# Optimization experiments

Hardware: AMD Instinct MI355X
Metric: run time of the kernel (lower is better)

The kernel has to match this reference:

```python
import jax, jax.numpy as jnp
import numpy as np
import math

B, H, S, D = 2, 16, 2048, 72
D12 = D // 12  # freq dim per head per component
L_PREFIX, L_SEQ = 576, 512
THETA_T = 100.0


def _make_freqs():
    n = H * D12
    log_min, log_max = math.log(math.pi), math.log(10.0 * math.pi)
    f = jnp.exp(jnp.linspace(log_min, log_max, n + 1)[:-1])  # (H*D12,)
    freqs = jnp.stack([f, f]).reshape(2, D12, H)
    freqs = jnp.swapaxes(freqs, -1, -2)  # (2, H, D12)
    t = THETA_T ** (-jnp.arange(n, dtype=jnp.float32) / n)
    t_freqs = t.reshape(D12, H).T  # (H, D12)
    return freqs.astype(jnp.float32), t_freqs.astype(jnp.float32)


def setup_inputs() -> dict:
    key = jax.random.key(0)
    ks = jax.random.split(key, 8)
    freqs, t_freqs = _make_freqs()
    return {
        "q": jax.random.normal(ks[0], (B, H, S, D), dtype=jnp.float32),
        "k": jax.random.normal(ks[1], (B, H, S, D), dtype=jnp.float32),
        "v": jax.random.normal(ks[2], (B, H, S, D), dtype=jnp.float32),
        "pos": jax.random.uniform(ks[3], (B, S, 2), dtype=jnp.float32),
        "pos_orig": jax.random.uniform(ks[4], (B, S, 2), dtype=jnp.float32),
        "time": jax.random.uniform(ks[5], (B, S), dtype=jnp.float32),
        "freqs": freqs,
        "t_freqs": t_freqs,
        "scale": jax.random.uniform(ks[6], (H, 1, 1), dtype=jnpp_f32()) if False else jax.random.uniform(ks[6], (H, 1, 1), dtype=jnp.float32) + 0.5,
        "l_prefix": L_PREFIX,
        "l_seq": L_SEQ,
    }


def jnp_f32():
    return jnp.float32


def _fp_rope_theta(pos, pos_orig, time, freqs, t_freqs):
    # FPRoPE.forward: theta per token, per head. (B,S,H,5*D12)
    p = jnp.stack([pos_orig, pos], axis=2) * 2.0 - 1.0  # (B,S,2,2)
    th_w = p[..., 0][:, :, :, None, None] * freqs[0]  # (B,S,2,H,D12)
    th_h = p[..., 1][:, :, :, None, None] * freqs[1]  # (B,S,2,H,D12)
    th_t = time[:, :, None, None, None] * t_freqs      # (B,S,1,H,D12)
    theta = jnp.concatenate([th_h, th_w, th_t], axis=2)  # (B,S,5,H,D12)
    theta = jnp.transpose(theta, (0, 3, 1, 2, 4)).reshape(B, H, S, 5 * D12)
    return theta


def _apply_rotary(x, theta):
    d = theta.shape[-1]
    x1, x2, x3 = x[..., :d], x[..., d:2 * d], x[..., 2 * d:]
    c, s = jnp.cos(theta), jnp.sin(theta)
    return jnp.concatenate([x1 * c - x2 * s, x2 * c + x1 * s, x3], axis=-1)


def _block_mask(l_prefix, l_seq):
    # inference_query_causal_mask_mod: prefix attends to nothing; pokes causal;
    # queries attend to prefix+pokes (and self via qn==kn).
    idx = jnp.arange(S)
    qn = (idx - l_prefix)[:, None]
    kn = (idx - l_prefix)[None, :]
    return (qn >= 0) & ((qn == kn) | ((qn >= kn) & (qn < l_seq)) | ((kn < l_seq) & (qn >= l_seq)))


def reference(q, k, v, pos, pos_orig, time, freqs, t_freqs, scale, l_prefix, l_seq):
    theta = _fp_rope_theta(pos, pos_orig, time, freqs, t_freqs)
    q = _apply_rotary(q, theta)
    k = _apply_rotary(k, theta)
    # cosine-similarity QK rescaling (scale_for_cosine_sim)
    eps = 1e-6
    ss = jnp.sqrt(scale)  # (H,1,1) broadcasts over (B,H,S,1)
    q = q * (ss * jax.lax.rsqrt(jnp.sum(q * q, axis=-1, keepdims=True) + eps))
    k = k * (ss * jax.lax.rsqrt(jnp.sum(k * k, axis=-1, keepdims=True) + eps))
    mask = _block_mask(l_prefix, l_seq)  # (S,S)
    scores = jnp.einsum('bhqd,bhkd->bhqk', q, k)
    scores = jnp.where(mask, scores, jnp.float32(-1e30))
    probs = jax.nn.softmax(scores, axis=-1)
    # fully-masked rows (prefix queries) output zeros, matching flex_attention
    row_valid = jnp.any(mask, axis=-1)  # (S,)
    probs = jnp.where(row_valid[None, None, :, None], probs, 0.0)
    return jnp.einsum('bhqk,bhkd->bhqd', probs, v)
```

## Files before the change

### kernel.cpp

```cpp
#include <hip/hip_runtime.h>
#include <math.h>

#define B_ 2
#define H_ 16
#define S_ 2048
#define D_ 72
#define LP 576
#define WEND 1088
#define DP 96
#define DV 80

#define KS 50
#define VS 33
#define PW 33
#define VBASE (64 * KS)
#define PBASE (VBASE + DV * VS)
#define LDSW (PBASE + 4 * 16 * PW)

#define NPREP2 (B_ * H_ * S_ / 8)
#define NVT    (32 * B_ * H_)

typedef __bf16 bf16x8 __attribute__((ext_vector_type(8)));
typedef float f32x4 __attribute__((ext_vector_type(4)));

static __device__ __forceinline__ unsigned pack2bf(float a, float b) {
    __bf16 x = (__bf16)a, y = (__bf16)b;
    unsigned short ux = __builtin_bit_cast(unsigned short, x);
    unsigned short uy = __builtin_bit_cast(unsigned short, y);
    return (unsigned)ux | ((unsigned)uy << 16);
}

static __device__ __forceinline__ f32x4 mfma16(bf16x8 a, bf16x8 b, f32x4 c) {
    return __builtin_amdgcn_mfma_f32_16x16x32_bf16(a, b, c, 0, 0, 0);
}

__global__ __launch_bounds__(256) void pre_kernel(
    const float* __restrict__ q, const float* __restrict__ k,
    const float* __restrict__ v,
    const float* __restrict__ pos, const float* __restrict__ pos_orig,
    const float* __restrict__ time_, const float* __restrict__ freqs,
    const float* __restrict__ t_freqs, const float* __restrict__ scale,
    unsigned* __restrict__ qn, unsigned* __restrict__ kn,
    unsigned short* __restrict__ vt, float* __restrict__ out)
{
    __shared__ float tile[64 * 77];
    if (blockIdx.x < NPREP2) {
        const int wave = threadIdx.x >> 6;
        const int lane = threadIdx.x & 63;
        const int j = lane & 31;
        const int row = blockIdx.x * 8 + wave * 2 + (lane >> 5);
        const int s = row & (S_ - 1);
        const int h = (row >> 11) & (H_ - 1);
        const int b = row >> 15;
        const long base = (long)row * D_;
        const int p2 = (b * S_ + s) * 2;

        float oq1 = 0.f, oq2 = 0.f, ok1 = 0.f, ok2 = 0.f;
        float pq[6], pk[6];
        float ssq = 0.f, ssk = 0.f;
        if (j < 30) {
            const float x1q = q[base + j], x2q = q[base + j + 30];
            const float x1k = k[base + j], x2k = k[base + j + 30];
            const int g = j / 6, i = j - 6 * g;
            const float fh = freqs[96 + h * 6 + i];
            const float fw = freqs[h * 6 + i];
            const float ft = t_freqs[h * 6 + i];
            const float f  = (g < 2) ? fh : ((g < 4) ? fw : ft);
            const float by_o = pos_orig[p2 + 1] * 2.f - 1.f;
            const float by_p = pos[p2 + 1]      * 2.f - 1.f;
            const float bx_o = pos_orig[p2 + 0] * 2.f - 1.f;
            const float bx_p = pos[p2 + 0]      * 2.f - 1.f;
            const float bt   = time_[b * S_ + s];
            const float bv = (g == 0) ? by_o : (g == 1) ? by_p :
                             (g == 2) ? bx_o : (g == 3) ? bx_p : bt;
            float sn, cs;
            __sincosf(bv * f, &sn, &cs);
            oq1 = x1q * cs - x2q * sn;  oq2 = x2q * cs + x1q * sn;
            ok1 = x1k * cs - x2k * sn;  ok2 = x2k * cs + x1k * sn;
            ssq = oq1 * oq1 + oq2 * oq2;
            ssk = ok1 * ok1 + ok2 * ok2;
        } else {
            const int e0 = 60 + 6 * (j - 30);
            #pragma unroll
            for (int m = 0; m < 3; ++m) {
                const float2 a = *(const float2*)(q + base + e0 + 2 * m);
                const float2 c = *(const float2*)(k + base + e0 + 2 * m);
                pq[2 * m] = a.x; pq[2 * m + 1] = a.y;
                pk[2 * m] = c.x; pk[2 * m + 1] = c.y;
                ssq += a.x * a.x + a.y * a.y;
                ssk += c.x * c.x + c.y * c.y;
            }
        }
        #pragma unroll
        for (int m = 1; m < 32; m <<= 1) { ssq += __shfl_xor(ssq, m); ssk += __shfl_xor(ssk, m); }
        const float ss = sqrtf(scale[h]);
        const float fq = ss * rsqrtf(ssq + 1e-6f);
        const float fk = ss * rsqrtf(ssk + 1e-6f);

        unsigned short* qs = (unsigned short*)qn;
        unsigned short* ks = (unsigned short*)kn;
        const long rb = (long)row * DP;
        if (j < 30) {
            qs[rb + j]      = __builtin_bit_cast(unsigned short, (__bf16)(oq1 * fq));
            qs[rb + j + 30] = __builtin_bit_cast(unsigned short, (__bf16)(oq2 * fq));
            ks[rb + j]      = __builtin_bit_cast(unsigned short, (__bf16)(ok1 * fk));
            ks[rb + j + 30] = __builtin_bit_cast(unsigned short, (__bf16)(ok2 * fk));
            if (j >= 26 && j < 29) {
                const uint4 z = make_uint4(0u, 0u, 0u, 0u);
                *(uint4*)(qn + row * 48 + 36 + (j - 26) * 4) = z;
                *(uint4*)(kn + row * 48 + 36 + (j - 26) * 4) = z;
            }
        } else {
            const int u0 = row * 48 + 30 + 3 * (j - 30);
            #pragma unroll
            for (int m = 0; m < 3; ++m) {
                qn[u0 + m] = pack2bf(pq[2 * m] * fq, pq[2 * m + 1] * fq);
                kn[u0 + m] = pack2bf(pk[2 * m] * fk, pk[2 * m + 1] * fk);
            }
        }
    } else {
        const int bx2 = blockIdx.x - NPREP2;
        const int st = bx2 & 31, bh = bx2 >> 5;
        const int s0 = st * 64;
        const int t = threadIdx.x;
        if (st < 9) {
            float4* o4 = (float4*)(out + (long)(bh * S_ + s0) * D_);
            for (int i = t; i < 1152; i += 256) o4[i] = make_float4(0.f, 0.f, 0.f, 0.f);
        }
        for (int i = t; i < 1152; i += 256) {
            const int r = i / 18, c = i - r * 18;
            const float4 g = ((const float4*)v)[((long)(bh * S_ + s0 + r) * 18) + c];
            float* d = &tile[r * 77 + c * 4];
            d[0] = g.x; d[1] = g.y; d[2] = g.z; d[3] = g.w;
        }
        __syncthreads();
        for (int i = t; i < 1280; i += 256) {
            const int dd = i >> 4, s4 = i & 15;
            float f0 = 0.f, f1 = 0.f, f2 = 0.f, f3 = 0.f;
            if (dd < D_) {
                f0 = tile[(s4 * 4 + 0) * 77 + dd];
                f1 = tile[(s4 * 4 + 1) * 77 + dd];
                f2 = tile[(s4 * 4 + 2) * 77 + dd];
                f3 = tile[(s4 * 4 + 3) * 77 + dd];
            }
            uint2 o; o.x = pack2bf(f0, f1); o.y = pack2bf(f2, f3);
            ((uint2*)vt)[((((long)bh * DV + dd) << 11) + s0 + s4 * 4) >> 2] = o;
        }
    }
}

__global__ __launch_bounds__(256) void attn_kernel(
    const unsigned short* __restrict__ qn, const unsigned short* __restrict__ kn,
    const unsigned short* __restrict__ vt, float* __restrict__ out)
{
    __shared__ __align__(16) unsigned lds[LDSW];
    const int bh = blockIdx.y;
    const int q0 = LP + blockIdx.x * 64;
    const int tid = threadIdx.x;
    const int w = tid >> 6, lane = tid & 63;
    const int quad = lane >> 4, l16 = lane & 15;
    const int q0w = q0 + 16 * w;
    const bool causal = (q0 < WEND);
    const int ntiles = causal ? (q0 >> 6) + 1 : (WEND >> 6);

    const unsigned short* qn_b = qn + (((long)bh) << 11) * DP;
    const unsigned short* kn_b = kn + (((long)bh) << 11) * DP;
    const unsigned short* vt_b = vt + (long)bh * DV * S_;

    bf16x8 qf[3];
    #pragma unroll
    for (int c = 0; c < 3; ++c)
        qf[c] = *(const bf16x8*)(qn_b + (long)(q0w + l16) * DP + c * 32 + quad * 8);

    f32x4 o[5];
    float den[4];
    #pragma unroll
    for (int dt = 0; dt < 5; ++dt) { o[dt][0]=0.f; o[dt][1]=0.f; o[dt][2]=0.f; o[dt][3]=0.f; }
    #pragma unroll
    for (int r = 0; r < 4; ++r) den[r] = 0.f;

    unsigned* Ps = lds + PBASE + w * (16 * PW);

    for (int kt = 0; kt < ntiles; ++kt) {
        const int k0 = kt * 64;
        __syncthreads();
        #pragma unroll
        for (int ii = 0; ii < 3; ++ii) {
            const int i = tid + ii * 256;
            const int r = i / 12, seg = i - r * 12;
            const int key = k0 + 32 * (r >> 5) + 2 * (r & 15) + ((r >> 4) & 1);
            *(uint4*)(lds + r * KS + seg * 4) = *(const uint4*)(kn_b + (long)key * DP + seg * 8);
        }
        for (int i = tid; i < 640; i += 256) {
            const int rr = i >> 3, seg = i & 7;
            *(uint4*)(lds + VBASE + rr * VS + seg * 4) =
                *(const uint4*)(vt_b + (((long)rr) << 11) + k0 + seg * 8);
        }
        __syncthreads();

        f32x4 acc[4];
        #pragma unroll
        for (int G = 0; G < 4; ++G) { acc[G][0]=0.f; acc[G][1]=0.f; acc[G][2]=0.f; acc[G][3]=0.f; }
        #pragma unroll
        for (int c = 0; c < 3; ++c)
            #pragma unroll
            for (int G = 0; G < 4; ++G) {
                const bf16x8 kf = *(const bf16x8*)(lds + (16 * G + l16) * KS + c * 16 + quad * 4);
                acc[G] = mfma16(qf[c], kf, acc[G]);
            }
        #pragma unroll
        for (int g2 = 0; g2 < 2; ++g2) {
            const int kb = k0 + 32 * g2 + 2 * l16;
            #pragma unroll
            for (int r = 0; r < 4; ++r) {
                const int qa = q0w + quad * 4 + r;
                float p0 = acc[2 * g2][r], p1 = acc[2 * g2 + 1][r];
                p0 = (!causal || kb     <= qa) ? __expf(p0) : 0.f;
                p1 = (!causal || kb + 1 <= qa) ? __expf(p1) : 0.f;
                const __bf16 pb0 = (__bf16)p0, pb1 = (__bf16)p1;
                den[r] += (float)pb0 + (float)pb1;
                Ps[(quad * 4 + r) * PW + g2 * 16 + l16] =
                    (unsigned)__builtin_bit_cast(unsigned short, pb0) |
                    ((unsigned)__builtin_bit_cast(unsigned short, pb1) << 16);
            }
        }
        const bf16x8 pa0 = *(const bf16x8*)(Ps + l16 * PW + quad * 4);
        const bf16x8 pa1 = *(const bf16x8*)(Ps + l16 * PW + 16 + quad * 4);
        #pragma unroll
        for (int dt = 0; dt < 5; ++dt) {
            const bf16x8 vf0 = *(const bf16x8*)(lds + VBASE + (dt * 16 + l16) * VS + quad * 4);
            const bf16x8 vf1 = *(const bf16x8*)(lds + VBASE + (dt * 16 + l16) * VS + 16 + quad * 4);
            o[dt] = mfma16(pa0, vf0, o[dt]);
            o[dt] = mfma16(pa1, vf1, o[dt]);
        }
    }

    #pragma unroll
    for (int r = 0; r < 4; ++r)
        #pragma unroll
        for (int x = 1; x < 16; x <<= 1) den[r] += __shfl_xor(den[r], x);

    if (!causal) {
        float* PsD = (float*)Ps;
        float sp = 0.f;
        #pragma unroll
        for (int c = 0; c < 3; ++c) {
            const bf16x8 kd = *(const bf16x8*)(kn_b + (long)(q0w + l16) * DP + c * 32 + quad * 8);
            #pragma unroll
            for (int j = 0; j < 8; ++j) sp += (float)qf[c][j] * (float)kd[j];
        }
        sp += __shfl_xor(sp, 16);
        sp += __shfl_xor(sp, 32);
        if (quad == 0) PsD[l16] = __expf(sp);
        #pragma unroll
        for (int r = 0; r < 4; ++r) {
            const float pd = PsD[quad * 4 + r];
            den[r] += pd;
            const int qa = q0w + quad * 4 + r;
            #pragma unroll
            for (int dt = 0; dt < 5; ++dt) {
                const unsigned short uv = vt_b[(((long)(dt * 16 + l16)) << 11) + qa];
                o[dt][r] += pd * (float)__builtin_bit_cast(__bf16, uv);
            }
        }
    }

    #pragma unroll
    for (int r = 0; r < 4; ++r) {
        const float inv = 1.f / den[r];
        const int qa = q0w + quad * 4 + r;
        float* orow = out + ((long)(bh * S_ + qa)) * D_;
        #pragma unroll
        for (int dt = 0; dt < 5; ++dt) {
            const int dim = dt * 16 + l16;
            if (dim < D_) orow[dim] = o[dt][r] * inv;
        }
    }
}

extern "C" void kernel_launch(void* const* d_in, const int* in_sizes, int n_in,
                              void* d_out, int out_size, void* d_ws, size_t ws_size,
                              hipStream_t stream) {
    const float* q        = (const float*)d_in[0];
    const float* k        = (const float*)d_in[1];
    const float* v        = (const float*)d_in[2];
    const float* pos      = (const float*)d_in[3];
    const float* pos_orig = (const float*)d_in[4];
    const float* time_    = (const float*)d_in[5];
    const float* freqs    = (const float*)d_in[6];
    const float* t_freqs  = (const float*)d_in[7];
    const float* scale    = (const float*)d_in[8];
    float* out = (float*)d_out;

    unsigned* qn = (unsigned*)d_ws;
    unsigned* kn = qn + (size_t)B_ * H_ * S_ * 48;
    unsigned short* vt = (unsigned short*)(kn + (size_t)B_ * H_ * S_ * 48);

    pre_kernel<<<dim3(NPREP2 + NVT), dim3(256), 0, stream>>>(
        q, k, v, pos, pos_orig, time_, freqs, t_freqs, scale, qn, kn, vt, out);
    attn_kernel<<<dim3((S_ - LP) / 64, B_ * H_), dim3(256), 0, stream>>>(
        (const unsigned short*)qn, (const unsigned short*)kn, vt, out);
}
```

Measured before the change: 193.4 us.

## Split attention key tiles across two blocks and add combine kernel

The attention grid gains a z dimension of 2, so each block handles every other key tile. Unnormalized partial outputs and denominators go to workspace, and a new combine kernel sums the two halves and normalizes. This doubles the number of blocks to balance the uneven causal workloads and fill more CUs, at the cost of an extra launch and extra global traffic. Separately, the pre kernel now stages the bf16 q/k rows in LDS and writes them out as coalesced 16-byte stores, with the zero padding folded into those stores.

```diff
diff --git a/kernel.cpp b/kernel.cpp
--- a/kernel.cpp
+++ b/kernel.cpp
@@ -9,6 +9,7 @@
 #define WEND 1088
 #define DP 96
 #define DV 80
+#define NQ (S_ - LP)
 
 #define KS 50
 #define VS 33
@@ -43,12 +44,14 @@
     unsigned* __restrict__ qn, unsigned* __restrict__ kn,
     unsigned short* __restrict__ vt, float* __restrict__ out)
 {
-    __shared__ float tile[64 * 77];
+    __shared__ __align__(16) float tile[64 * 77];
     if (blockIdx.x < NPREP2) {
+        unsigned short* shp = (unsigned short*)tile;
         const int wave = threadIdx.x >> 6;
         const int lane = threadIdx.x & 63;
         const int j = lane & 31;
-        const int row = blockIdx.x * 8 + wave * 2 + (lane >> 5);
+        const int rw = wave * 2 + (lane >> 5);
+        const int row = blockIdx.x * 8 + rw;
         const int s = row & (S_ - 1);
         const int h = (row >> 11) & (H_ - 1);
         const int b = row >> 15;
@@ -97,26 +100,30 @@
         const float fq = ss * rsqrtf(ssq + 1e-6f);
         const float fk = ss * rsqrtf(ssk + 1e-6f);
 
-        unsigned short* qs = (unsigned short*)qn;
-        unsigned short* ks = (unsigned short*)kn;
-        const long rb = (long)row * DP;
+        unsigned short* sq_ = shp + rw * 96;
+        unsigned short* sk_ = shp + 768 + rw * 96;
         if (j < 30) {
-            qs[rb + j]      = __builtin_bit_cast(unsigned short, (__bf16)(oq1 * fq));
-            qs[rb + j + 30] = __builtin_bit_cast(unsigned short, (__bf16)(oq2 * fq));
-            ks[rb + j]      = __builtin_bit_cast(unsigned short, (__bf16)(ok1 * fk));
-            ks[rb + j + 30] = __builtin_bit_cast(unsigned short, (__bf16)(ok2 * fk));
-            if (j >= 26 && j < 29) {
-                const uint4 z = make_uint4(0u, 0u, 0u, 0u);
-                *(uint4*)(qn + row * 48 + 36 + (j - 26) * 4) = z;
-                *(uint4*)(kn + row * 48 + 36 + (j - 26) * 4) = z;
-            }
+            sq_[j]      = __builtin_bit_cast(unsigned short, (__bf16)(oq1 * fq));
+            sq_[j + 30] = __builtin_bit_cast(unsigned short, (__bf16)(oq2 * fq));
+            sk_[j]      = __builtin_bit_cast(unsigned short, (__bf16)(ok1 * fk));
+            sk_[j + 30] = __builtin_bit_cast(unsigned short, (__bf16)(ok2 * fk));
         } else {
-            const int u0 = row * 48 + 30 + 3 * (j - 30);
-            #pragma unroll
-            for (int m = 0; m < 3; ++m) {
-                qn[u0 + m] = pack2bf(pq[2 * m] * fq, pq[2 * m + 1] * fq);
-                kn[u0 + m] = pack2bf(pk[2 * m] * fk, pk[2 * m + 1] * fk);
-            }
+            const int e0 = 60 + 6 * (j - 30);
+            #pragma unroll
+            for (int m = 0; m < 6; ++m) {
+                sq_[e0 + m] = __builtin_bit_cast(unsigned short, (__bf16)(pq[m] * fq));
+                sk_[e0 + m] = __builtin_bit_cast(unsigned short, (__bf16)(pk[m] * fk));
+            }
+        }
+        __syncthreads();
+        const int t = threadIdx.x;
+        if (t < 192) {
+            const int arr = t / 96, rem = t - arr * 96;
+            const int rr = rem / 12, seg = rem - rr * 12;
+            uint4 val = make_uint4(0u, 0u, 0u, 0u);
+            if (seg < 9) val = ((const uint4*)(shp + arr * 768 + rr * 96))[seg];
+            unsigned* dst = (arr ? kn : qn) + ((long)(blockIdx.x * 8 + rr)) * 48;
+            ((uint4*)dst)[seg] = val;
         }
     } else {
         const int bx2 = blockIdx.x - NPREP2;
@@ -151,10 +158,12 @@
 
 __global__ __launch_bounds__(256) void attn_kernel(
     const unsigned short* __restrict__ qn, const unsigned short* __restrict__ kn,
-    const unsigned short* __restrict__ vt, float* __restrict__ out)
+    const unsigned short* __restrict__ vt,
+    float* __restrict__ po, float* __restrict__ pden)
 {
     __shared__ __align__(16) unsigned lds[LDSW];
     const int bh = blockIdx.y;
+    const int kz = blockIdx.z;
     const int q0 = LP + blockIdx.x * 64;
     const int tid = threadIdx.x;
     const int w = tid >> 6, lane = tid & 63;
@@ -181,7 +190,7 @@
 
     unsigned* Ps = lds + PBASE + w * (16 * PW);
 
-    for (int kt = 0; kt < ntiles; ++kt) {
+    for (int kt = kz; kt < ntiles; kt += 2) {
         const int k0 = kt * 64;
         __syncthreads();
         #pragma unroll
@@ -240,7 +249,7 @@
         #pragma unroll
         for (int x = 1; x < 16; x <<= 1) den[r] += __shfl_xor(den[r], x);
 
-    if (!causal) {
+    if (kz == 1 && !causal) {
         float* PsD = (float*)Ps;
         float sp = 0.f;
         #pragma unroll
@@ -265,16 +274,36 @@
         }
     }
 
+    const long pobase = ((long)(kz * 32 + bh)) * NQ * DV;
+    const long pdbase = ((long)(kz * 32 + bh)) * NQ;
     #pragma unroll
     for (int r = 0; r < 4; ++r) {
-        const float inv = 1.f / den[r];
-        const int qa = q0w + quad * 4 + r;
-        float* orow = out + ((long)(bh * S_ + qa)) * D_;
-        #pragma unroll
-        for (int dt = 0; dt < 5; ++dt) {
-            const int dim = dt * 16 + l16;
-            if (dim < D_) orow[dim] = o[dt][r] * inv;
-        }
+        const int rq = blockIdx.x * 64 + 16 * w + quad * 4 + r;
+        #pragma unroll
+        for (int dt = 0; dt < 5; ++dt)
+            po[pobase + (long)rq * DV + dt * 16 + l16] = o[dt][r];
+        if (l16 == 0) pden[pdbase + rq] = den[r];
+    }
+}
+
+__global__ __launch_bounds__(256) void combine_kernel(
+    const float* __restrict__ po, const float* __restrict__ pden,
+    float* __restrict__ out)
+{
+    const int t = threadIdx.x;
+    const int rowid = blockIdx.x * 16 + (t >> 4);
+    const int d0 = t & 15;
+    const int bh = rowid / NQ;
+    const int rq = rowid - bh * NQ;
+    const long p0 = ((long)bh) * NQ * DV + (long)rq * DV;
+    const long p1 = ((long)(32 + bh)) * NQ * DV + (long)rq * DV;
+    const float den = pden[(long)bh * NQ + rq] + pden[(long)(32 + bh) * NQ + rq];
+    const float inv = 1.f / den;
+    float* orow = out + ((long)bh * S_ + LP + rq) * D_;
+    #pragma unroll
+    for (int j = 0; j < 5; ++j) {
+        const int d = d0 + 16 * j;
+        if (d < D_) orow[d] = (po[p0 + d] + po[p1 + d]) * inv;
     }
 }
 
@@ -295,9 +324,12 @@
     unsigned* qn = (unsigned*)d_ws;
     unsigned* kn = qn + (size_t)B_ * H_ * S_ * 48;
     unsigned short* vt = (unsigned short*)(kn + (size_t)B_ * H_ * S_ * 48);
+    float* po = (float*)(vt + (size_t)B_ * H_ * DV * S_);
+    float* pden = po + (size_t)2 * B_ * H_ * NQ * DV;
 
     pre_kernel<<<dim3(NPREP2 + NVT), dim3(256), 0, stream>>>(
         q, k, v, pos, pos_orig, time_, freqs, t_freqs, scale, qn, kn, vt, out);
-    attn_kernel<<<dim3((S_ - LP) / 64, B_ * H_), dim3(256), 0, stream>>>(
-        (const unsigned short*)qn, (const unsigned short*)kn, vt, out);
-}
+    attn_kernel<<<dim3(NQ / 64, B_ * H_, 2), dim3(256), 0, stream>>>(
+        (const unsigned short*)qn, (const unsigned short*)kn, vt, po, pden);
+    combine_kernel<<<dim3(B_ * H_ * NQ / 16), dim3(256), 0, stream>>>(po, pden, out);
+}
```

After: 199.3 us. 1.03x slower.

## Shrink attention key tile to 32 and stage prep output through shared memory

Applied to the files above, without the earlier changes.

The attention loop now processes 32 keys per iteration instead of 64. For causal blocks this trims the masked work on the diagonal tile, and it shrinks the LDS footprint, but it doubles the number of loop iterations and barriers. The prep kernel now writes normalized bf16 q/k rows into shared memory first, then emits them with coalesced 16-byte stores that include the zero padding, replacing scattered 2-byte global stores. The extra __syncthreads is placed in a branch that is uniform per block.

```diff
diff --git a/kernel.cpp b/kernel.cpp
--- a/kernel.cpp
+++ b/kernel.cpp
@@ -9,11 +9,12 @@
 #define WEND 1088
 #define DP 96
 #define DV 80
-
-#define KS 50
-#define VS 33
-#define PW 33
-#define VBASE (64 * KS)
+#define NQ (S_ - LP)
+
+#define KS 49
+#define VS 17
+#define PW 17
+#define VBASE (32 * KS)
 #define PBASE (VBASE + DV * VS)
 #define LDSW (PBASE + 4 * 16 * PW)
 
@@ -43,12 +44,14 @@
     unsigned* __restrict__ qn, unsigned* __restrict__ kn,
     unsigned short* __restrict__ vt, float* __restrict__ out)
 {
-    __shared__ float tile[64 * 77];
+    __shared__ __align__(16) float tile[64 * 77];
     if (blockIdx.x < NPREP2) {
+        unsigned short* shp = (unsigned short*)tile;
         const int wave = threadIdx.x >> 6;
         const int lane = threadIdx.x & 63;
         const int j = lane & 31;
-        const int row = blockIdx.x * 8 + wave * 2 + (lane >> 5);
+        const int rw = wave * 2 + (lane >> 5);
+        const int row = blockIdx.x * 8 + rw;
         const int s = row & (S_ - 1);
         const int h = (row >> 11) & (H_ - 1);
         const int b = row >> 15;
@@ -97,26 +100,30 @@
         const float fq = ss * rsqrtf(ssq + 1e-6f);
         const float fk = ss * rsqrtf(ssk + 1e-6f);
 
-        unsigned short* qs = (unsigned short*)qn;
-        unsigned short* ks = (unsigned short*)kn;
-        const long rb = (long)row * DP;
+        unsigned short* sq_ = shp + rw * 96;
+        unsigned short* sk_ = shp + 768 + rw * 96;
         if (j < 30) {
-            qs[rb + j]      = __builtin_bit_cast(unsigned short, (__bf16)(oq1 * fq));
-            qs[rb + j + 30] = __builtin_bit_cast(unsigned short, (__bf16)(oq2 * fq));
-            ks[rb + j]      = __builtin_bit_cast(unsigned short, (__bf16)(ok1 * fk));
-            ks[rb + j + 30] = __builtin_bit_cast(unsigned short, (__bf16)(ok2 * fk));
-            if (j >= 26 && j < 29) {
-                const uint4 z = make_uint4(0u, 0u, 0u, 0u);
-                *(uint4*)(qn + row * 48 + 36 + (j - 26) * 4) = z;
-                *(uint4*)(kn + row * 48 + 36 + (j - 26) * 4) = z;
-            }
+            sq_[j]      = __builtin_bit_cast(unsigned short, (__bf16)(oq1 * fq));
+            sq_[j + 30] = __builtin_bit_cast(unsigned short, (__bf16)(oq2 * fq));
+            sk_[j]      = __builtin_bit_cast(unsigned short, (__bf16)(ok1 * fk));
+            sk_[j + 30] = __builtin_bit_cast(unsigned short, (__bf16)(ok2 * fk));
         } else {
-            const int u0 = row * 48 + 30 + 3 * (j - 30);
-            #pragma unroll
-            for (int m = 0; m < 3; ++m) {
-                qn[u0 + m] = pack2bf(pq[2 * m] * fq, pq[2 * m + 1] * fq);
-                kn[u0 + m] = pack2bf(pk[2 * m] * fk, pk[2 * m + 1] * fk);
-            }
+            const int e0 = 60 + 6 * (j - 30);
+            #pragma unroll
+            for (int m = 0; m < 6; ++m) {
+                sq_[e0 + m] = __builtin_bit_cast(unsigned short, (__bf16)(pq[m] * fq));
+                sk_[e0 + m] = __builtin_bit_cast(unsigned short, (__bf16)(pk[m] * fk));
+            }
+        }
+        __syncthreads();
+        const int t = threadIdx.x;
+        if (t < 192) {
+            const int arr = t / 96, rem = t - arr * 96;
+            const int rr = rem / 12, seg = rem - rr * 12;
+            uint4 val = make_uint4(0u, 0u, 0u, 0u);
+            if (seg < 9) val = ((const uint4*)(shp + arr * 768 + rr * 96))[seg];
+            unsigned* dst = (arr ? kn : qn) + ((long)(blockIdx.x * 8 + rr)) * 48;
+            ((uint4*)dst)[seg] = val;
         }
     } else {
         const int bx2 = blockIdx.x - NPREP2;
@@ -161,7 +168,7 @@
     const int quad = lane >> 4, l16 = lane & 15;
     const int q0w = q0 + 16 * w;
     const bool causal = (q0 < WEND);
-    const int ntiles = causal ? (q0 >> 6) + 1 : (WEND >> 6);
+    const int ntiles = causal ? ((q0 + 63) >> 5) + 1 : (WEND >> 5);
 
     const unsigned short* qn_b = qn + (((long)bh) << 11) * DP;
     const unsigned short* kn_b = kn + (((long)bh) << 11) * DP;
@@ -182,56 +189,52 @@
     unsigned* Ps = lds + PBASE + w * (16 * PW);
 
     for (int kt = 0; kt < ntiles; ++kt) {
-        const int k0 = kt * 64;
+        const int k0 = kt * 32;
         __syncthreads();
         #pragma unroll
         for (int ii = 0; ii < 3; ++ii) {
             const int i = tid + ii * 256;
-            const int r = i / 12, seg = i - r * 12;
-            const int key = k0 + 32 * (r >> 5) + 2 * (r & 15) + ((r >> 4) & 1);
-            *(uint4*)(lds + r * KS + seg * 4) = *(const uint4*)(kn_b + (long)key * DP + seg * 8);
-        }
-        for (int i = tid; i < 640; i += 256) {
-            const int rr = i >> 3, seg = i & 7;
-            *(uint4*)(lds + VBASE + rr * VS + seg * 4) =
-                *(const uint4*)(vt_b + (((long)rr) << 11) + k0 + seg * 8);
+            if (i < 384) {
+                const int r = i / 12, seg = i - r * 12;
+                const int key = k0 + 2 * (r & 15) + (r >> 4);
+                *(uint4*)(lds + r * KS + seg * 4) = *(const uint4*)(kn_b + (long)key * DP + seg * 8);
+            } else if (i < 704) {
+                const int j = i - 384;
+                const int rr = j >> 2, seg = j & 3;
+                *(uint4*)(lds + VBASE + rr * VS + seg * 4) =
+                    *(const uint4*)(vt_b + (((long)rr) << 11) + k0 + seg * 8);
+            }
         }
         __syncthreads();
 
-        f32x4 acc[4];
-        #pragma unroll
-        for (int G = 0; G < 4; ++G) { acc[G][0]=0.f; acc[G][1]=0.f; acc[G][2]=0.f; acc[G][3]=0.f; }
+        f32x4 acc[2];
+        #pragma unroll
+        for (int G = 0; G < 2; ++G) { acc[G][0]=0.f; acc[G][1]=0.f; acc[G][2]=0.f; acc[G][3]=0.f; }
         #pragma unroll
         for (int c = 0; c < 3; ++c)
             #pragma unroll
-            for (int G = 0; G < 4; ++G) {
+            for (int G = 0; G < 2; ++G) {
                 const bf16x8 kf = *(const bf16x8*)(lds + (16 * G + l16) * KS + c * 16 + quad * 4);
                 acc[G] = mfma16(qf[c], kf, acc[G]);
             }
-        #pragma unroll
-        for (int g2 = 0; g2 < 2; ++g2) {
-            const int kb = k0 + 32 * g2 + 2 * l16;
-            #pragma unroll
-            for (int r = 0; r < 4; ++r) {
-                const int qa = q0w + quad * 4 + r;
-                float p0 = acc[2 * g2][r], p1 = acc[2 * g2 + 1][r];
-                p0 = (!causal || kb     <= qa) ? __expf(p0) : 0.f;
-                p1 = (!causal || kb + 1 <= qa) ? __expf(p1) : 0.f;
-                const __bf16 pb0 = (__bf16)p0, pb1 = (__bf16)p1;
-                den[r] += (float)pb0 + (float)pb1;
-                Ps[(quad * 4 + r) * PW + g2 * 16 + l16] =
-                    (unsigned)__builtin_bit_cast(unsigned short, pb0) |
-                    ((unsigned)__builtin_bit_cast(unsigned short, pb1) << 16);
-            }
-        }
-        const bf16x8 pa0 = *(const bf16x8*)(Ps + l16 * PW + quad * 4);
-        const bf16x8 pa1 = *(const bf16x8*)(Ps + l16 * PW + 16 + quad * 4);
+        const int kb = k0 + 2 * l16;
+        #pragma unroll
+        for (int r = 0; r < 4; ++r) {
+            const int qa = q0w + quad * 4 + r;
+            float p0 = acc[0][r], p1 = acc[1][r];
+            p0 = (!causal || kb     <= qa) ? __expf(p0) : 0.f;
+            p1 = (!causal || kb + 1 <= qa) ? __expf(p1) : 0.f;
+            const __bf16 pb0 = (__bf16)p0, pb1 = (__bf16)p1;
+            den[r] += (float)pb0 + (float)pb1;
+            Ps[(quad * 4 + r) * PW + l16] =
+                (unsigned)__builtin_bit_cast(unsigned short, pb0) |
+                ((unsigned)__builtin_bit_cast(unsigned short, pb1) << 16);
+        }
+        const bf16x8 pa = *(const bf16x8*)(Ps + l16 * PW + quad * 4);
         #pragma unroll
         for (int dt = 0; dt < 5; ++dt) {
-            const bf16x8 vf0 = *(const bf16x8*)(lds + VBASE + (dt * 16 + l16) * VS + quad * 4);
-            const bf16x8 vf1 = *(const bf16x8*)(lds + VBASE + (dt * 16 + l16) * VS + 16 + quad * 4);
-            o[dt] = mfma16(pa0, vf0, o[dt]);
-            o[dt] = mfma16(pa1, vf1, o[dt]);
+            const bf16x8 vf = *(const bf16x8*)(lds + VBASE + (dt * 16 + l16) * VS + quad * 4);
+            o[dt] = mfma16(pa, vf, o[dt]);
         }
     }
 
@@ -298,6 +301,6 @@
 
     pre_kernel<<<dim3(NPREP2 + NVT), dim3(256), 0, stream>>>(
         q, k, v, pos, pos_orig, time_, freqs, t_freqs, scale, qn, kn, vt, out);
-    attn_kernel<<<dim3((S_ - LP) / 64, B_ * H_), dim3(256), 0, stream>>>(
+    attn_kernel<<<dim3(NQ / 64, B_ * H_), dim3(256), 0, stream>>>(
         (const unsigned short*)qn, (const unsigned short*)kn, vt, out);
 }
```

New measurement: 200.5 us. 1.04x slower.
